# Optimization experiments

Hardware: AMD Instinct MI355X
Metric: run time of the kernel (lower is better)

The kernel has to match this reference:

```python
import jax, jax.numpy as jnp
import numpy as np
from jax import lax

KS = [3, 3, 3, 5, 5, 7, 7, 7, 9, 9, 11, 11]  # deterministic sorted draw from [3,5,7,9,11], k=12
B, L, OUT_CH = 32, 262144, 4
EPS = 1e-5


def setup_inputs() -> dict:
    key = jax.random.key(0)
    ks = jax.random.split(key, 8 + len(KS))
    inp = {
        "x": jax.random.normal(ks[0], (B, 1, L), jnp.float32),
        "w1": jax.random.normal(ks[1], (128, 256), jnp.float32) * 0.0625,
        "b1": jnp.zeros((128,), jnp.float32),
        "w2": jax.random.normal(ks[2], (12, 128), jnp.float32) * 0.088,
        "b2": jnp.zeros((12,), jnp.float32),
        "bn_gamma": jnp.ones((OUT_CH,), jnp.float32),
        "bn_beta": jnp.zeros((OUT_CH,), jnp.float32),
    }
    for i, k in enumerate(KS):
        inp[f"k{i}"] = jax.random.normal(ks[8 + i], (OUT_CH, 1, k), jnp.float32)
    return inp


def reference(x, w1, b1, w2, b2, bn_gamma, bn_beta,
              k0, k1, k2, k3, k4, k5, k6, k7, k8, k9, k10, k11):
    kernels = [k0, k1, k2, k3, k4, k5, k6, k7, k8, k9, k10, k11]
    b, _, n = x.shape
    # Attention: AdaptiveAvgPool1d(256) -> Linear -> ReLU -> Linear -> softmax(dim=2)
    pooled = x.reshape(b, 1, 256, n // 256).mean(-1)            # [B,1,256]
    h = jax.nn.relu(jnp.einsum('bcd,hd->bch', pooled, w1) + b1)  # [B,1,128]
    y = jax.nn.softmax(jnp.einsum('bch,fh->bcf', h, w2) + b2, axis=2)  # [B,1,12]
    s = y[0, 0]  # scalar weight per filter (faithful to y[0][0][i] in source)

    max_len = n - KS[0] + 1
    out = jnp.zeros((b, OUT_CH, max_len), x.dtype)
    for i, k in enumerate(kernels):
        c = lax.conv_general_dilated(x, k * s[i], (1,), 'VALID',
                                     dimension_numbers=('NCH', 'OIH', 'NCH'))
        out = out.at[:, :, :c.shape[-1]].add(c)  # right-pad-with-zeros then add

    # BatchNorm1d in training mode: batch stats over (N, L), biased variance
    mean = out.mean(axis=(0, 2), keepdims=True)
    var = ((out - mean) ** 2).mean(axis=(0, 2), keepdims=True)
    out = (out - mean) * lax.rsqrt(var + EPS)
    out = out * bn_gamma[None, :, None] + bn_beta[None, :, None]
    return jax.nn.relu(out)
```

## Files before the change

kernel.cpp:

```cpp
#include <hip/hip_runtime.h>

#define L_LEN   262144
#define OUT_LEN 262142
#define BATCH   32
#define NTOT    (32.0 * 262142.0)

typedef float v4f __attribute__((ext_vector_type(4)));

struct KPtrs { const float* p[12]; };

__global__ __launch_bounds__(256, 4) void stats_pool_kernel(const float* __restrict__ x,
                                                            float* __restrict__ part,
                                                            float* __restrict__ pooled) {
    __shared__ float xt[2064];
    __shared__ float wsum[4];
    int tid = threadIdx.x;
    float X = 0.0f, R[11];
    #pragma unroll
    for (int l = 0; l < 11; ++l) R[l] = 0.0f;

    for (int it = 0; it < 4; ++it) {
        int T = blockIdx.x * 4 + it;
        int row = T >> 7, seg = T & 127;
        int base = seg << 11;
        const float* xb = x + row * L_LEN;
        *(float4*)&xt[4 * tid]        = *(const float4*)(xb + base + 4 * tid);
        *(float4*)&xt[1024 + 4 * tid] = *(const float4*)(xb + base + 1024 + 4 * tid);
        if (tid < 3) {
            float4 v = {0.f, 0.f, 0.f, 0.f};
            if (seg < 127) v = *(const float4*)(xb + base + 2048 + 4 * tid);
            *(float4*)&xt[2048 + 4 * tid] = v;
        }
        __syncthreads();

        float xv[18];
        const float4* xr = (const float4*)&xt[8 * tid];
        #pragma unroll
        for (int i = 0; i < 4; ++i) {
            float4 a = xr[i];
            xv[4*i] = a.x; xv[4*i+1] = a.y; xv[4*i+2] = a.z; xv[4*i+3] = a.w;
        }
        float2 a4 = *(const float2*)&xt[8 * tid + 16];
        xv[16] = a4.x; xv[17] = a4.y;

        float s8 = 0.0f;
        #pragma unroll
        for (int p = 0; p < 8; ++p) s8 += xv[p];
        X += s8;
        #pragma unroll
        for (int l = 0; l < 11; ++l) {
            float r = 0.0f;
            #pragma unroll
            for (int p = 0; p < 8; ++p) r = fmaf(xv[p], xv[p + l], r);
            R[l] += r;
        }

        if (blockIdx.x < 32) {
            float ps = s8;
            #pragma unroll
            for (int off = 32; off; off >>= 1) ps += __shfl_down(ps, off);
            if ((tid & 63) == 0) wsum[tid >> 6] = ps;
            __syncthreads();
            if (tid == 0) {
                pooled[blockIdx.x * 8 + 2 * it]     = (wsum[0] + wsum[1]) * (1.0f / 1024.0f);
                pooled[blockIdx.x * 8 + 2 * it + 1] = (wsum[2] + wsum[3]) * (1.0f / 1024.0f);
            }
        }
        __syncthreads();
    }

    #pragma unroll
    for (int off = 32; off; off >>= 1) {
        X += __shfl_down(X, off);
        #pragma unroll
        for (int l = 0; l < 11; ++l) R[l] += __shfl_down(R[l], off);
    }
    __shared__ float red[4][12];
    int wave = tid >> 6;
    if ((tid & 63) == 0) {
        red[wave][0] = X;
        #pragma unroll
        for (int l = 0; l < 11; ++l) red[wave][1 + l] = R[l];
    }
    __syncthreads();
    if (tid < 12)
        part[tid * 1024 + blockIdx.x] = red[0][tid] + red[1][tid] + red[2][tid] + red[3][tid];
}

__global__ void attn_finalize_kernel(const float* __restrict__ w1, const float* __restrict__ b1,
                                     const float* __restrict__ w2, const float* __restrict__ b2,
                                     KPtrs kp, const float* __restrict__ pooled,
                                     const float* __restrict__ part,
                                     const float* __restrict__ gamma, const float* __restrict__ beta,
                                     float* __restrict__ Kscl, float* __restrict__ biasv) {
    __shared__ float h[128];
    __shared__ float logits[12];
    __shared__ float s[12];
    __shared__ float Kr[220];
    __shared__ double vals[12];
    __shared__ float g[4];
    int tid = threadIdx.x;
    int w = tid >> 6, lane = tid & 63;

    float4 pv = ((const float4*)pooled)[lane];
    for (int i = 0; i < 8; ++i) {
        int t = w * 8 + i;
        float4 wv = ((const float4*)(w1 + t * 256))[lane];
        float p = wv.x * pv.x + wv.y * pv.y + wv.z * pv.z + wv.w * pv.w;
        #pragma unroll
        for (int off = 32; off; off >>= 1) p += __shfl_down(p, off);
        if (lane == 0) h[t] = fmaxf(p + b1[t], 0.0f);
    }
    __syncthreads();
    if (w < 12) {
        float2 wv = ((const float2*)(w2 + w * 128))[lane];
        float p = wv.x * h[2 * lane] + wv.y * h[2 * lane + 1];
        #pragma unroll
        for (int off = 32; off; off >>= 1) p += __shfl_down(p, off);
        if (lane == 0) logits[w] = p + b2[w];
    }
    __syncthreads();
    if (tid == 0) {
        float m = logits[0];
        #pragma unroll
        for (int i = 1; i < 12; ++i) m = fmaxf(m, logits[i]);
        float e[12]; float sum = 0.0f;
        #pragma unroll
        for (int i = 0; i < 12; ++i) { e[i] = expf(logits[i] - m); sum += e[i]; }
        float inv = 1.0f / sum;
        #pragma unroll
        for (int i = 0; i < 12; ++i) s[i] = e[i] * inv;
    }
    __syncthreads();
    constexpr int KSa[12] = {3,3,3,5,5,7,7,7,9,9,11,11};
    if (tid < 220) {
        int q = tid / 44, r = tid % 44, c = r / 11, j = r % 11;
        int kmax = 2 * q + 3;
        float v = 0.0f;
        #pragma unroll
        for (int i = 0; i < 12; ++i) {
            int k = KSa[i];
            if (k <= kmax && j < k) v = fmaf(s[i], kp.p[i][c * k + j], v);
        }
        Kr[tid] = v;
    }
    if (w < 12) {
        double d = 0.0;
        #pragma unroll 4
        for (int i = 0; i < 16; ++i) d += (double)part[w * 1024 + i * 64 + lane];
        #pragma unroll
        for (int off = 32; off; off >>= 1) d += __shfl_down(d, off);
        if (lane == 0) vals[w] = d;
    }
    __syncthreads();
    if (tid < 4) {
        int c = tid;
        const float* Kc = Kr + 4 * 44 + c * 11;
        double sK = 0.0;
        for (int j = 0; j < 11; ++j) sK += (double)Kc[j];
        double mean = sK * vals[0] / NTOT;
        double ex2 = 0.0;
        for (int l = 0; l < 11; ++l) {
            double A = 0.0;
            for (int j = 0; j + l < 11; ++j) A += (double)Kc[j] * (double)Kc[j + l];
            ex2 += (l ? 2.0 : 1.0) * A * vals[1 + l];
        }
        ex2 /= NTOT;
        double var = ex2 - mean * mean;
        float gg = gamma[c] * (float)(1.0 / sqrt(var + 1e-5));
        g[c] = gg;
        biasv[c] = beta[c] - (float)mean * gg;
    }
    __syncthreads();
    if (tid < 220) {
        int c = (tid / 11) % 4;
        Kscl[tid] = Kr[tid] * g[c];
    }
}

__global__ __launch_bounds__(256, 4) void write_kernel(const float* __restrict__ x,
                                                       const float* __restrict__ Kscl,
                                                       const float* __restrict__ biasv,
                                                       float* __restrict__ out) {
    __shared__ float xt[2064];
    int tid = threadIdx.x;
    int b = blockIdx.x >> 7, seg = blockIdx.x & 127;
    int base = seg << 11;
    const float* xb = x + b * L_LEN;

    *(float4*)&xt[4 * tid]        = *(const float4*)(xb + base + 4 * tid);
    *(float4*)&xt[1024 + 4 * tid] = *(const float4*)(xb + base + 1024 + 4 * tid);
    if (tid < 4) {
        float4 v = {0.f, 0.f, 0.f, 0.f};
        if (seg < 127) v = *(const float4*)(xb + base + 2048 + 4 * tid);
        *(float4*)&xt[2048 + 4 * tid] = v;
    }

    float K[4][11], bias[4];
    #pragma unroll
    for (int c = 0; c < 4; ++c) {
        #pragma unroll
        for (int j = 0; j < 11; ++j) K[c][j] = Kscl[4 * 44 + c * 11 + j];
        bias[c] = biasv[c];
    }
    __syncthreads();

    #pragma unroll
    for (int gdx = 0; gdx < 2; ++gdx) {
        int lt = gdx * 1024 + 4 * tid;
        bool scalar = (seg == 127) && (gdx == 1) && (tid >= 253);
        if (!scalar) {
            float xv[16];
            const float4* xr = (const float4*)&xt[lt];
            #pragma unroll
            for (int i = 0; i < 4; ++i) {
                float4 a = xr[i];
                xv[4*i] = a.x; xv[4*i+1] = a.y; xv[4*i+2] = a.z; xv[4*i+3] = a.w;
            }
            #pragma unroll
            for (int c = 0; c < 4; ++c) {
                int sh = (c & 1) ? 2 : 0;
                float v[4];
                #pragma unroll
                for (int p = 0; p < 4; ++p) {
                    float a = bias[c];
                    #pragma unroll
                    for (int j = 0; j < 11; ++j) a = fmaf(K[c][j], xv[sh + p + j], a);
                    v[p] = fmaxf(a, 0.0f);
                }
                float* op = out + (size_t)(4 * b + c) * OUT_LEN + base + sh + lt;
                *(v4f*)op = (v4f){v[0], v[1], v[2], v[3]};
            }
        } else {
            #pragma unroll
            for (int par = 0; par < 2; ++par) {
                int sh = 2 * par;
                for (int p = 0; p < 4; ++p) {
                    int t = base + sh + lt + p;
                    if (t >= OUT_LEN) continue;
                    int rem = L_LEN - t;
                    int q = (rem - 3) >> 1; if (q > 4) q = 4;
                    int kmax = 2 * q + 3;
                    int li = sh + lt + p;
                    for (int c = par; c < 4; c += 2) {
                        float a = bias[c];
                        for (int j = 0; j < kmax; ++j) a = fmaf(Kscl[q * 44 + c * 11 + j], xt[li + j], a);
                        out[(size_t)(4 * b + c) * OUT_LEN + t] = fmaxf(a, 0.0f);
                    }
                }
            }
        }
    }
    if (seg == 0 && tid == 0) {
        for (int c = 1; c < 4; c += 2) {
            for (int t = 0; t < 2; ++t) {
                float a = bias[c];
                #pragma unroll
                for (int j = 0; j < 11; ++j) a = fmaf(K[c][j], xt[t + j], a);
                out[(size_t)(4 * b + c) * OUT_LEN + t] = fmaxf(a, 0.0f);
            }
        }
    }
}

extern "C" void kernel_launch(void* const* d_in, const int* in_sizes, int n_in,
                              void* d_out, int out_size, void* d_ws, size_t ws_size,
                              hipStream_t stream) {
    const float* x     = (const float*)d_in[0];
    const float* w1    = (const float*)d_in[1];
    const float* b1    = (const float*)d_in[2];
    const float* w2    = (const float*)d_in[3];
    const float* b2    = (const float*)d_in[4];
    const float* gamma = (const float*)d_in[5];
    const float* beta  = (const float*)d_in[6];
    KPtrs kp;
    for (int i = 0; i < 12; ++i) kp.p[i] = (const float*)d_in[7 + i];
    float* out = (float*)d_out;

    char* ws = (char*)d_ws;
    float* pooled = (float*)(ws + 0);
    float* Kscl   = (float*)(ws + 1024);
    float* biasv  = (float*)(ws + 2048);
    float* part   = (float*)(ws + 4096);

    stats_pool_kernel<<<dim3(1024), dim3(256), 0, stream>>>(x, part, pooled);
    attn_finalize_kernel<<<dim3(1), dim3(1024), 0, stream>>>(w1, b1, w2, b2, kp, pooled,
                                                             part, gamma, beta, Kscl, biasv);
    write_kernel<<<dim3(4096), dim3(256), 0, stream>>>(x, Kscl, biasv, out);
}
```

Baseline: 65.30 us.

## Split pooling into its own kernel and overlap attention MLP with stats pass

Pooling of the first batch row moves into a small separate kernel. The attention MLP, softmax and kernel mixing then run in an extra block of the stats kernel, so they overlap with the autocorrelation statistics pass. The single-block finalize kernel is reduced to the BN fold on 256 threads. This shortens the serial single-block critical path, at the cost of one extra kernel launch plus an extra small pass over x.

```diff
diff --git a/kernel.cpp b/kernel.cpp
--- a/kernel.cpp
+++ b/kernel.cpp
@@ -9,12 +9,84 @@
 
 struct KPtrs { const float* p[12]; };
 
-__global__ __launch_bounds__(256, 4) void stats_pool_kernel(const float* __restrict__ x,
-                                                            float* __restrict__ part,
-                                                            float* __restrict__ pooled) {
+__global__ void pool_kernel(const float* __restrict__ x, float* __restrict__ pooled) {
+    int bin = blockIdx.x;
+    int tid = threadIdx.x;
+    const float4* x4 = (const float4*)(x + bin * 1024);
+    float4 v = x4[tid];
+    float sum = v.x + v.y + v.z + v.w;
+    #pragma unroll
+    for (int off = 32; off; off >>= 1) sum += __shfl_down(sum, off);
+    __shared__ float wred[4];
+    int wave = tid >> 6;
+    if ((tid & 63) == 0) wred[wave] = sum;
+    __syncthreads();
+    if (tid == 0)
+        pooled[bin] = (wred[0] + wred[1] + wred[2] + wred[3]) * (1.0f / 1024.0f);
+}
+
+__global__ __launch_bounds__(256, 4) void stats_mlp_kernel(const float* __restrict__ x,
+                                                           const float* __restrict__ w1,
+                                                           const float* __restrict__ b1,
+                                                           const float* __restrict__ w2,
+                                                           const float* __restrict__ b2,
+                                                           KPtrs kp,
+                                                           const float* __restrict__ pooled,
+                                                           float* __restrict__ part,
+                                                           float* __restrict__ Kraw) {
+    int tid = threadIdx.x;
+
+    if (blockIdx.x == 1024) {
+        __shared__ float h[128];
+        __shared__ float logits[12];
+        __shared__ float s[12];
+        int w = tid >> 6, lane = tid & 63;
+        float4 pv = ((const float4*)pooled)[lane];
+        for (int i = 0; i < 32; ++i) {
+            int t = w * 32 + i;
+            float4 wv = ((const float4*)(w1 + t * 256))[lane];
+            float p = wv.x * pv.x + wv.y * pv.y + wv.z * pv.z + wv.w * pv.w;
+            #pragma unroll
+            for (int off = 32; off; off >>= 1) p += __shfl_down(p, off);
+            if (lane == 0) h[t] = fmaxf(p + b1[t], 0.0f);
+        }
+        __syncthreads();
+        for (int f = w; f < 12; f += 4) {
+            float2 wv = ((const float2*)(w2 + f * 128))[lane];
+            float p = wv.x * h[2 * lane] + wv.y * h[2 * lane + 1];
+            #pragma unroll
+            for (int off = 32; off; off >>= 1) p += __shfl_down(p, off);
+            if (lane == 0) logits[f] = p + b2[f];
+        }
+        __syncthreads();
+        if (tid == 0) {
+            float m = logits[0];
+            #pragma unroll
+            for (int i = 1; i < 12; ++i) m = fmaxf(m, logits[i]);
+            float e[12]; float sum = 0.0f;
+            #pragma unroll
+            for (int i = 0; i < 12; ++i) { e[i] = expf(logits[i] - m); sum += e[i]; }
+            float inv = 1.0f / sum;
+            #pragma unroll
+            for (int i = 0; i < 12; ++i) s[i] = e[i] * inv;
+        }
+        __syncthreads();
+        constexpr int KSa[12] = {3,3,3,5,5,7,7,7,9,9,11,11};
+        if (tid < 220) {
+            int q = tid / 44, r = tid % 44, c = r / 11, j = r % 11;
+            int kmax = 2 * q + 3;
+            float v = 0.0f;
+            #pragma unroll
+            for (int i = 0; i < 12; ++i) {
+                int k = KSa[i];
+                if (k <= kmax && j < k) v = fmaf(s[i], kp.p[i][c * k + j], v);
+            }
+            Kraw[tid] = v;
+        }
+        return;
+    }
+
     __shared__ float xt[2064];
-    __shared__ float wsum[4];
-    int tid = threadIdx.x;
     float X = 0.0f, R[11];
     #pragma unroll
     for (int l = 0; l < 11; ++l) R[l] = 0.0f;
@@ -54,18 +126,6 @@
             for (int p = 0; p < 8; ++p) r = fmaf(xv[p], xv[p + l], r);
             R[l] += r;
         }
-
-        if (blockIdx.x < 32) {
-            float ps = s8;
-            #pragma unroll
-            for (int off = 32; off; off >>= 1) ps += __shfl_down(ps, off);
-            if ((tid & 63) == 0) wsum[tid >> 6] = ps;
-            __syncthreads();
-            if (tid == 0) {
-                pooled[blockIdx.x * 8 + 2 * it]     = (wsum[0] + wsum[1]) * (1.0f / 1024.0f);
-                pooled[blockIdx.x * 8 + 2 * it + 1] = (wsum[2] + wsum[3]) * (1.0f / 1024.0f);
-            }
-        }
         __syncthreads();
     }
 
@@ -87,70 +147,23 @@
         part[tid * 1024 + blockIdx.x] = red[0][tid] + red[1][tid] + red[2][tid] + red[3][tid];
 }
 
-__global__ void attn_finalize_kernel(const float* __restrict__ w1, const float* __restrict__ b1,
-                                     const float* __restrict__ w2, const float* __restrict__ b2,
-                                     KPtrs kp, const float* __restrict__ pooled,
-                                     const float* __restrict__ part,
-                                     const float* __restrict__ gamma, const float* __restrict__ beta,
-                                     float* __restrict__ Kscl, float* __restrict__ biasv) {
-    __shared__ float h[128];
-    __shared__ float logits[12];
-    __shared__ float s[12];
+__global__ void fold_kernel(const float* __restrict__ part,
+                            const float* __restrict__ Kraw,
+                            const float* __restrict__ gamma, const float* __restrict__ beta,
+                            float* __restrict__ Kscl, float* __restrict__ biasv) {
+    __shared__ double vals[12];
     __shared__ float Kr[220];
-    __shared__ double vals[12];
     __shared__ float g[4];
     int tid = threadIdx.x;
     int w = tid >> 6, lane = tid & 63;
-
-    float4 pv = ((const float4*)pooled)[lane];
-    for (int i = 0; i < 8; ++i) {
-        int t = w * 8 + i;
-        float4 wv = ((const float4*)(w1 + t * 256))[lane];
-        float p = wv.x * pv.x + wv.y * pv.y + wv.z * pv.z + wv.w * pv.w;
-        #pragma unroll
-        for (int off = 32; off; off >>= 1) p += __shfl_down(p, off);
-        if (lane == 0) h[t] = fmaxf(p + b1[t], 0.0f);
-    }
-    __syncthreads();
-    if (w < 12) {
-        float2 wv = ((const float2*)(w2 + w * 128))[lane];
-        float p = wv.x * h[2 * lane] + wv.y * h[2 * lane + 1];
-        #pragma unroll
-        for (int off = 32; off; off >>= 1) p += __shfl_down(p, off);
-        if (lane == 0) logits[w] = p + b2[w];
-    }
-    __syncthreads();
-    if (tid == 0) {
-        float m = logits[0];
-        #pragma unroll
-        for (int i = 1; i < 12; ++i) m = fmaxf(m, logits[i]);
-        float e[12]; float sum = 0.0f;
-        #pragma unroll
-        for (int i = 0; i < 12; ++i) { e[i] = expf(logits[i] - m); sum += e[i]; }
-        float inv = 1.0f / sum;
-        #pragma unroll
-        for (int i = 0; i < 12; ++i) s[i] = e[i] * inv;
-    }
-    __syncthreads();
-    constexpr int KSa[12] = {3,3,3,5,5,7,7,7,9,9,11,11};
-    if (tid < 220) {
-        int q = tid / 44, r = tid % 44, c = r / 11, j = r % 11;
-        int kmax = 2 * q + 3;
-        float v = 0.0f;
-        #pragma unroll
-        for (int i = 0; i < 12; ++i) {
-            int k = KSa[i];
-            if (k <= kmax && j < k) v = fmaf(s[i], kp.p[i][c * k + j], v);
-        }
-        Kr[tid] = v;
-    }
-    if (w < 12) {
+    if (tid < 220) Kr[tid] = Kraw[tid];
+    for (int v = w; v < 12; v += 4) {
         double d = 0.0;
         #pragma unroll 4
-        for (int i = 0; i < 16; ++i) d += (double)part[w * 1024 + i * 64 + lane];
+        for (int i = 0; i < 16; ++i) d += (double)part[v * 1024 + i * 64 + lane];
         #pragma unroll
         for (int off = 32; off; off >>= 1) d += __shfl_down(d, off);
-        if (lane == 0) vals[w] = d;
+        if (lane == 0) vals[v] = d;
     }
     __syncthreads();
     if (tid < 4) {
@@ -279,12 +292,14 @@
 
     char* ws = (char*)d_ws;
     float* pooled = (float*)(ws + 0);
-    float* Kscl   = (float*)(ws + 1024);
-    float* biasv  = (float*)(ws + 2048);
+    float* Kraw   = (float*)(ws + 1024);
+    float* Kscl   = (float*)(ws + 2048);
+    float* biasv  = (float*)(ws + 3072);
     float* part   = (float*)(ws + 4096);
 
-    stats_pool_kernel<<<dim3(1024), dim3(256), 0, stream>>>(x, part, pooled);
-    attn_finalize_kernel<<<dim3(1), dim3(1024), 0, stream>>>(w1, b1, w2, b2, kp, pooled,
-                                                             part, gamma, beta, Kscl, biasv);
+    pool_kernel<<<dim3(256), dim3(256), 0, stream>>>(x, pooled);
+    stats_mlp_kernel<<<dim3(1025), dim3(256), 0, stream>>>(x, w1, b1, w2, b2, kp,
+                                                           pooled, part, Kraw);
+    fold_kernel<<<dim3(1), dim3(256), 0, stream>>>(part, Kraw, gamma, beta, Kscl, biasv);
     write_kernel<<<dim3(4096), dim3(256), 0, stream>>>(x, Kscl, biasv, out);
 }
```

Result: slower. 83.99 us (+28.6%).
